# Kernel optimization log

Hardware: AMD Instinct MI355X
Metric: run time of the kernel (lower is better)

## Reference

```python
import jax, jax.numpy as jnp
import numpy as np

# Mamba2 defaults with d_model=512, headdim=2*d_model (=> nheads=1)
D_MODEL = 512
D_INNER = 2 * D_MODEL          # expand=2
D_STATE = 128
NHEADS = 1                     # d_inner // headdim = 1
HEADDIM = D_INNER              # headdim = 2*hidden_dim
D_CONV = 4
NG = 1                         # ngroups
EPS = 1e-5


def setup_inputs() -> dict:
    key = jax.random.key(0)
    ks = jax.random.split(key, 8)
    B, L = 4, 2048
    d_in_proj = 2 * D_INNER + 2 * NG * D_STATE + NHEADS   # 2305
    conv_ch = D_INNER + 2 * NG * D_STATE                  # 1280
    x = jax.random.normal(ks[0], (B, L, D_MODEL), jnp.float32)
    rnn_state = jax.random.normal(ks[1], (B, D_MODEL), jnp.float32)
    W_in = jax.random.normal(ks[2], (d_in_proj, D_MODEL), jnp.float32) * (D_MODEL ** -0.5)
    conv_w = jax.random.normal(ks[3], (conv_ch, 1, D_CONV), jnp.float32) * (D_CONV ** -0.5)
    conv_b = jnp.zeros((conv_ch,), jnp.float32)
    # dt_bias = inv_softplus(dt) with dt ~ U(1e-3, 0.1), as in Mamba2 init
    dt = jax.random.uniform(ks[4], (NHEADS,), jnp.float32, 1e-3, 0.1)
    dt_bias = jnp.log(jnp.expm1(dt))
    A_log = jnp.log(jax.random.uniform(ks[5], (NHEADS,), jnp.float32, 1.0, 16.0))
    Dp = jnp.ones((NHEADS,), jnp.float32)
    norm_w = jnp.ones((D_INNER,), jnp.float32)
    W_out = jax.random.normal(ks[6], (D_MODEL, D_INNER), jnp.float32) * (D_INNER ** -0.5)
    return dict(x=x, rnn_state=rnn_state, W_in=W_in, conv_w=conv_w, conv_b=conv_b,
                dt_bias=dt_bias, A_log=A_log, Dp=Dp, norm_w=norm_w, W_out=W_out)


def _mamba2(x, W_in, conv_w, conv_b, dt_bias, A_log, Dp, norm_w, W_out):
    B, L, _ = x.shape
    zxbcdt = jnp.einsum('bld,ed->ble', x, W_in)           # (B,L,2305)
    z, xBC, dt = jnp.split(zxbcdt, [D_INNER, 2 * D_INNER + 2 * NG * D_STATE], axis=-1)
    # causal depthwise conv1d over channels (B,C,L), then silu
    xBC = xBC.transpose(0, 2, 1)
    xBC = jax.lax.conv_general_dilated(
        xBC, conv_w, window_strides=(1,), padding=[(D_CONV - 1, 0)],
        feature_group_count=xBC.shape[1], dimension_numbers=('NCH', 'OIH', 'NCH'))
    xBC = jax.nn.silu(xBC + conv_b[None, :, None]).transpose(0, 2, 1)
    xs, Bm, Cm = jnp.split(xBC, [D_INNER, D_INNER + NG * D_STATE], axis=-1)
    xs = xs.reshape(B, L, NHEADS, HEADDIM)
    dt = jax.nn.softplus(dt + dt_bias)                    # (B,L,H)
    A = -jnp.exp(A_log)                                   # (H,)
    dA = jnp.exp(dt * A)                                  # (B,L,H)

    # selective state-space scan: h_t = dA_t*h_{t-1} + dt_t * x_t (x) B_t ; y_t = h_t @ C_t
    def step(state, inp):
        x_t, dt_t, dA_t, B_t, C_t = inp
        state = dA_t[:, :, None, None] * state \
            + (dt_t[:, :, None] * x_t)[..., None] * B_t[:, None, None, :]
        y_t = jnp.einsum('bhpn,bn->bhp', state, C_t)
        return state, y_t

    init = jnp.zeros((B, NHEADS, HEADDIM, D_STATE), x.dtype)
    inputs = (xs.transpose(1, 0, 2, 3), dt.transpose(1, 0, 2), dA.transpose(1, 0, 2),
              Bm.transpose(1, 0, 2), Cm.transpose(1, 0, 2))
    _, ys = jax.lax.scan(step, init, inputs)              # (L,B,H,P)
    y = ys.transpose(1, 0, 2, 3) + Dp[None, None, :, None] * xs
    y = y.reshape(B, L, D_INNER)
    # gated RMSNorm (gate first, norm_before_gate=False)
    y = y * jax.nn.silu(z)
    y = y * jax.lax.rsqrt(jnp.mean(y * y, axis=-1, keepdims=True) + EPS) * norm_w
    return jnp.einsum('bld,od->blo', y, W_out)


def reference(x, rnn_state, W_in, conv_w, conv_b, dt_bias, A_log, Dp, norm_w, W_out):
    out = _mamba2(x, W_in, conv_w, conv_b, dt_bias, A_log, Dp, norm_w, W_out)
    return (out, rnn_state)
```

## Files before the change

kernel.cpp:

```cpp
#include <hip/hip_runtime.h>
#include <cstdint>
#include <cstddef>


typedef __bf16 bf16_t;
typedef __bf16 bf16x8 __attribute__((ext_vector_type(8)));
typedef __bf16 bf16x4 __attribute__((ext_vector_type(4)));
typedef __bf16 bf16x2 __attribute__((ext_vector_type(2)));
typedef float  f32x4  __attribute__((ext_vector_type(4)));

#define BATCH   4
#define SEQLEN  2048
#define MROWS   8192
#define DMODEL  512
#define DINNER  1024
#define DSTATE  128
#define NZX     2304
#define NCONV   1280
#define CHUNK   128
#define NCHUNK  16
#define NBC     64

__device__ __forceinline__ float siluf(float x) { return x / (1.f + __expf(-x)); }

__device__ __forceinline__ void load_lds16(const bf16_t* g, bf16_t* l)
{
    __builtin_amdgcn_global_load_lds(
        (const __attribute__((address_space(1))) void*)g,
        (__attribute__((address_space(3))) void*)l,
        16, 0, 0);
}

template <typename OutT>
__device__ __forceinline__ void gemm_body(
    const bf16_t* __restrict__ A, const bf16_t* __restrict__ B,
    OutT* __restrict__ C, int Ntot, int K, int lda, int ldb, int bn, int bm)
{
    __shared__ __align__(16) bf16_t As[128 * 64];
    __shared__ __align__(16) bf16_t Bs[128 * 64];

    const int tid  = threadIdx.x;
    const int wave = tid >> 6, lane = tid & 63;
    const int lr = lane & 15, q = lane >> 4;
    const int wm = (wave & 1) * 64, wn = (wave >> 1) * 64;

    f32x4 acc[4][4];
    #pragma unroll
    for (int i = 0; i < 4; ++i)
        #pragma unroll
        for (int j = 0; j < 4; ++j)
            acc[i][j] = (f32x4){0.f, 0.f, 0.f, 0.f};

    const int row_a0 = bm * 128, row_b0 = bn * 128;
    const int srow = tid >> 3;
    const int gsw  = (((tid & 7) ^ (srow & 7))) * 8;
    const int lsl  = (tid & 7) * 8;

    for (int kt = 0; kt < K; kt += 64) {
        #pragma unroll
        for (int i = 0; i < 4; ++i) {
            int row = srow + i * 32;
            load_lds16(&A[(size_t)(row_a0 + row) * lda + kt + gsw], &As[row * 64 + lsl]);
            load_lds16(&B[(size_t)(row_b0 + row) * ldb + kt + gsw], &Bs[row * 64 + lsl]);
        }
        __syncthreads();
        #pragma unroll
        for (int k0 = 0; k0 < 64; k0 += 32) {
            bf16x8 af[4], bfr[4];
            #pragma unroll
            for (int mi = 0; mi < 4; ++mi) {
                int r = wm + mi * 16 + lr, kc = (k0 >> 3) + q;
                af[mi] = *reinterpret_cast<const bf16x8*>(
                    &As[r * 64 + ((kc ^ (r & 7)) << 3)]);
            }
            #pragma unroll
            for (int ni = 0; ni < 4; ++ni) {
                int r = wn + ni * 16 + lr, kc = (k0 >> 3) + q;
                bfr[ni] = *reinterpret_cast<const bf16x8*>(
                    &Bs[r * 64 + ((kc ^ (r & 7)) << 3)]);
            }
            #pragma unroll
            for (int mi = 0; mi < 4; ++mi)
                #pragma unroll
                for (int ni = 0; ni < 4; ++ni)
                    acc[mi][ni] = __builtin_amdgcn_mfma_f32_16x16x32_bf16(
                        af[mi], bfr[ni], acc[mi][ni], 0, 0, 0);
        }
        __syncthreads();
    }

    #pragma unroll
    for (int mi = 0; mi < 4; ++mi)
        #pragma unroll
        for (int ni = 0; ni < 4; ++ni)
            #pragma unroll
            for (int ri = 0; ri < 4; ++ri) {
                int row = row_a0 + wm + mi * 16 + q * 4 + ri;
                int col = row_b0 + wn + ni * 16 + lr;
                C[(size_t)row * Ntot + col] = (OutT)acc[mi][ni][ri];
            }
}

template <typename OutT>
__global__ __launch_bounds__(256) void gemm_bt_kernel(
    const bf16_t* __restrict__ A, const bf16_t* __restrict__ B,
    OutT* __restrict__ C, int Ntot, int K, int lda, int ldb,
    size_t sA, size_t sB, size_t sC)
{
    gemm_body<OutT>(A + (size_t)blockIdx.z * sA, B + (size_t)blockIdx.z * sB,
                    C + (size_t)blockIdx.z * sC, Ntot, K, lda, ldb,
                    blockIdx.x, blockIdx.y);
}

__device__ __forceinline__ void cumsum_body(
    const float* __restrict__ dtv, const float* __restrict__ A_log,
    float* __restrict__ sarr, float* __restrict__ Pv,
    float* __restrict__ EdTv, float* __restrict__ chp, int bc)
{
    __shared__ float w0sum, stot;
    int j = threadIdx.x;
    bool active = j < CHUNK;
    int lane = j & 63;
    int r = bc * CHUNK + j;
    float A = -expf(A_log[0]);
    float dt = active ? dtv[r] : 0.f;
    float s = dt;
    #pragma unroll
    for (int m = 1; m <= 32; m <<= 1) {
        float o = __shfl_up(s, m);
        if (lane >= m) s += o;
    }
    if (j == 63) w0sum = s;
    __syncthreads();
    if (j >= 64 && active) s += w0sum;
    if (j == 127) stot = s;
    __syncthreads();
    if (active) {
        float sT = stot;
        sarr[r] = s;
        Pv[r]   = expf(A * s);
        EdTv[r] = expf(A * (sT - s)) * dt;
        if (j == 127) chp[bc] = expf(A * sT);
    }
}

__global__ __launch_bounds__(256) void gemm1_kernel(
    const bf16_t* __restrict__ xb, const bf16_t* __restrict__ winb,
    bf16_t* __restrict__ zx, const float* __restrict__ dtv,
    const float* __restrict__ A_log, float* __restrict__ sarr,
    float* __restrict__ Pv, float* __restrict__ EdTv, float* __restrict__ chp)
{
    int linear = blockIdx.x;
    if (linear < (NZX / 128) * (MROWS / 128)) {
        int xcd = linear & 7, j = linear >> 3;
        int bm = xcd * 8 + (j & 7);
        int bn = j >> 3;
        gemm_body<bf16_t>(xb, winb, zx, NZX, DMODEL, DMODEL, DMODEL, bn, bm);
    } else {
        cumsum_body(dtv, A_log, sarr, Pv, EdTv, chp, linear - 1152);
    }
}

__global__ __launch_bounds__(256) void gemm2_kernel(
    const bf16_t* __restrict__ yb, const bf16_t* __restrict__ woutb,
    float* __restrict__ out)
{
    int linear = blockIdx.x;
    int xcd = linear & 7, j = linear >> 3;
    int bm = xcd * 8 + (j & 7);
    int bn = j >> 3;
    gemm_body<float>(yb, woutb, out, DMODEL, DINNER, DINNER, DINNER, bn, bm);
}

__global__ __launch_bounds__(256) void gemm_y_kernel(
    const bf16_t* __restrict__ Mx, const bf16_t* __restrict__ Xt,
    const bf16_t* __restrict__ Stb, bf16_t* __restrict__ yf)
{
    __shared__ __align__(16) bf16_t As[128 * 64];
    __shared__ __align__(16) bf16_t Bs[128 * 64];

    const int bc = blockIdx.z, bn = blockIdx.x;
    const bf16_t* Ab = Mx + (size_t)bc * 32768;
    const bf16_t* Xb = Xt  + (size_t)bc * 131072 + (size_t)bn * 128 * 128;
    const bf16_t* Sb = Stb + (size_t)bc * 131072 + (size_t)bn * 128 * 128;
    bf16_t* Cb = yf + (size_t)bc * 131072;

    const int tid  = threadIdx.x;
    const int wave = tid >> 6, lane = tid & 63;
    const int lr = lane & 15, q = lane >> 4;
    const int wm = (wave & 1) * 64, wn = (wave >> 1) * 64;

    f32x4 acc[4][4];
    #pragma unroll
    for (int i = 0; i < 4; ++i)
        #pragma unroll
        for (int j = 0; j < 4; ++j)
            acc[i][j] = (f32x4){0.f, 0.f, 0.f, 0.f};

    const int srow = tid >> 3;
    const int gsw  = (((tid & 7) ^ (srow & 7))) * 8;
    const int lsl  = (tid & 7) * 8;

    for (int kt = 0; kt < 256; kt += 64) {
        const bf16_t* bsrc = (kt < 128) ? (Xb + kt) : (Sb + (kt - 128));
        #pragma unroll
        for (int i = 0; i < 4; ++i) {
            int row = srow + i * 32;
            load_lds16(&Ab[(size_t)row * 256 + kt + gsw], &As[row * 64 + lsl]);
            load_lds16(&bsrc[(size_t)row * 128 + gsw], &Bs[row * 64 + lsl]);
        }
        __syncthreads();
        #pragma unroll
        for (int k0 = 0; k0 < 64; k0 += 32) {
            bf16x8 af[4], bfr[4];
            #pragma unroll
            for (int mi = 0; mi < 4; ++mi) {
                int r = wm + mi * 16 + lr, kc = (k0 >> 3) + q;
                af[mi] = *reinterpret_cast<const bf16x8*>(
                    &As[r * 64 + ((kc ^ (r & 7)) << 3)]);
            }
            #pragma unroll
            for (int ni = 0; ni < 4; ++ni) {
                int r = wn + ni * 16 + lr, kc = (k0 >> 3) + q;
                bfr[ni] = *reinterpret_cast<const bf16x8*>(
                    &Bs[r * 64 + ((kc ^ (r & 7)) << 3)]);
            }
            #pragma unroll
            for (int mi = 0; mi < 4; ++mi)
                #pragma unroll
                for (int ni = 0; ni < 4; ++ni)
                    acc[mi][ni] = __builtin_amdgcn_mfma_f32_16x16x32_bf16(
                        af[mi], bfr[ni], acc[mi][ni], 0, 0, 0);
        }
        __syncthreads();
    }

    #pragma unroll
    for (int mi = 0; mi < 4; ++mi)
        #pragma unroll
        for (int ni = 0; ni < 4; ++ni)
            #pragma unroll
            for (int ri = 0; ri < 4; ++ri) {
                int row = wm + mi * 16 + q * 4 + ri;
                int col = bn * 128 + wn + ni * 16 + lr;
                Cb[(size_t)row * 1024 + col] = (bf16_t)acc[mi][ni][ri];
            }
}

__global__ __launch_bounds__(256) void dtcast_kernel(
    const float* __restrict__ x, const float* __restrict__ W_in,
    const float* __restrict__ dt_bias, const float* __restrict__ W_out,
    float* __restrict__ dtv, bf16_t* __restrict__ xb,
    bf16_t* __restrict__ winb, bf16_t* __restrict__ woutb)
{
    int bid = blockIdx.x;
    if (bid < MROWS / 4) {
        int wave = threadIdx.x >> 6, lane = threadIdx.x & 63;
        int r = bid * 4 + wave;
        const float* xr = x + (size_t)r * DMODEL + lane * 8;
        const float* wr = W_in + (size_t)NZX * DMODEL + lane * 8;
        float4 a0 = *reinterpret_cast<const float4*>(xr);
        float4 a1 = *reinterpret_cast<const float4*>(xr + 4);
        float4 b0 = *reinterpret_cast<const float4*>(wr);
        float4 b1 = *reinterpret_cast<const float4*>(wr + 4);

        bf16x8 xo;
        xo[0] = (bf16_t)a0.x; xo[1] = (bf16_t)a0.y; xo[2] = (bf16_t)a0.z; xo[3] = (bf16_t)a0.w;
        xo[4] = (bf16_t)a1.x; xo[5] = (bf16_t)a1.y; xo[6] = (bf16_t)a1.z; xo[7] = (bf16_t)a1.w;
        *reinterpret_cast<bf16x8*>(xb + (size_t)r * DMODEL + lane * 8) = xo;

        float s = a0.x * b0.x + a0.y * b0.y + a0.z * b0.z + a0.w * b0.w
                + a1.x * b1.x + a1.y * b1.y + a1.z * b1.z + a1.w * b1.w;
        #pragma unroll
        for (int m = 32; m >= 1; m >>= 1) s += __shfl_xor(s, m);
        if (lane == 0) {
            float t  = s + dt_bias[0];
            dtv[r] = (t > 20.f) ? t : log1pf(expf(t));
        }
        return;
    }
    int i = (bid - MROWS / 4) * 256 + threadIdx.x;
    const int n4a = 2305 * DMODEL / 4, n4b = DMODEL * DINNER / 4;
    const float* src; bf16_t* dst; int j;
    if (i < n4a)            { src = W_in;  dst = winb;  j = i; }
    else if (i < n4a + n4b) { src = W_out; dst = woutb; j = i - n4a; }
    else return;
    float4 v = reinterpret_cast<const float4*>(src)[j];
    bf16x4 o;
    o[0] = (bf16_t)v.x; o[1] = (bf16_t)v.y; o[2] = (bf16_t)v.z; o[3] = (bf16_t)v.w;
    reinterpret_cast<bf16x4*>(dst)[j] = o;
}

__global__ __launch_bounds__(256) void conv_tr_kernel(
    const bf16_t* __restrict__ zx, const float* __restrict__ cw,
    const float* __restrict__ cb, const float* __restrict__ EdTv,
    bf16_t* __restrict__ xbc, bf16_t* __restrict__ Xt, bf16_t* __restrict__ Bwt)
{
    constexpr int TS = 66;
    __shared__ bf16_t tile[128 * TS];
    __shared__ float cwS[64 * 4];
    __shared__ float cbS[64];

    int id  = blockIdx.x;
    int xcd = id & 7;
    int k   = id >> 3;
    int bc  = xcd * 8 + (k & 7);
    int rest = k >> 3;
    int cg   = rest >> 1;
    int half = rest & 1;
    int c0   = cg * 128 + half * 64;
    int tid  = threadIdx.x;

    if (tid < 64) {
        float4 w = *reinterpret_cast<const float4*>(cw + (size_t)(c0 + tid) * 4);
        *reinterpret_cast<float4*>(&cwS[tid * 4]) = w;
        cbS[tid] = cb[c0 + tid];
    }
    __syncthreads();

    int lrow = tid >> 3;
    int lc8  = (tid & 7) * 8;
    int g0 = bc * 128;

    #pragma unroll
    for (int pass = 0; pass < 4; ++pass) {
        int row = pass * 32 + lrow;
        int g = g0 + row;
        int l = g & (SEQLEN - 1);
        float acc[8];
        #pragma unroll
        for (int m = 0; m < 8; ++m) acc[m] = cbS[lc8 + m];
        #pragma unroll
        for (int kk = 0; kk < 4; ++kk) {
            if (l + kk >= 3) {
                bf16x8 v = *reinterpret_cast<const bf16x8*>(
                    zx + (size_t)(g + kk - 3) * NZX + DINNER + c0 + lc8);
                #pragma unroll
                for (int m = 0; m < 8; ++m)
                    acc[m] += cwS[(lc8 + m) * 4 + kk] * (float)v[m];
            }
        }
        bf16x8 o;
        #pragma unroll
        for (int m = 0; m < 8; ++m) o[m] = (bf16_t)siluf(acc[m]);
        *reinterpret_cast<bf16x8*>(xbc + (size_t)g * NCONV + c0 + lc8) = o;
        if (cg < 9) {
            #pragma unroll
            for (int jj = 0; jj < 4; ++jj) {
                bf16x2 p; p[0] = o[jj * 2]; p[1] = o[jj * 2 + 1];
                *reinterpret_cast<bf16x2*>(&tile[row * TS + lc8 + jj * 2]) = p;
            }
        }
    }
    if (cg == 9) return;
    __syncthreads();

    const bool isB = (cg == 8);
    int jo = (tid >> 4) * 8;
    int i  = tid & 15;
    float sc[8];
    #pragma unroll
    for (int m = 0; m < 8; ++m)
        sc[m] = isB ? EdTv[bc * 128 + jo + m] : 1.f;

    #pragma unroll
    for (int pass = 0; pass < 4; ++pass) {
        int oc = pass * 16 + i;
        bf16x8 o;
        #pragma unroll
        for (int m = 0; m < 8; ++m)
            o[m] = (bf16_t)((float)tile[(jo + m) * TS + oc] * sc[m]);
        bf16_t* dst = isB
            ? (Bwt + (size_t)bc * 16384 + (size_t)(c0 - 1024 + oc) * 128 + jo)
            : (Xt + (size_t)bc * 131072 + (size_t)(c0 + oc) * 128 + jo);
        *reinterpret_cast<bf16x8*>(dst) = o;
    }
}

__global__ __launch_bounds__(256) void scan_combine_kernel(
    const bf16_t* __restrict__ cstate, const float* __restrict__ chp,
    bf16_t* __restrict__ Stb)
{
    int idx = blockIdx.x * 256 + threadIdx.x;
    int b   = idx >> 17;
    int np  = idx & 131071;
    float v = 0.f;
    for (int c = 0; c < NCHUNK; ++c) {
        size_t off = ((size_t)(b * NCHUNK + c) << 17) + np;
        Stb[off] = (bf16_t)v;
        float tmp = (float)cstate[off];
        v = chp[b * NCHUNK + c] * v + tmp;
    }
}

__global__ __launch_bounds__(256) void mbuild_kernel(
    const float* __restrict__ sarr, const float* __restrict__ dtv,
    const float* __restrict__ Pv, const float* __restrict__ A_log,
    const bf16_t* __restrict__ xbc, bf16_t* __restrict__ Mx)
{
    __shared__ __align__(16) bf16_t Cs[128 * 128];
    __shared__ __align__(16) bf16_t Bs2[128 * 128];
    __shared__ float sj[CHUNK], dj[CHUNK], pj[CHUNK];

    int bc = blockIdx.x, tid = threadIdx.x;
    if (tid < CHUNK) {
        sj[tid] = sarr[bc * CHUNK + tid];
        dj[tid] = dtv[bc * CHUNK + tid];
        pj[tid] = Pv[bc * CHUNK + tid];
    }
    int rowbase = bc * 128;
    int srow = tid >> 4;
    int gsw  = (((tid & 15) ^ (srow & 7))) * 8;
    int lsl  = (tid & 15) * 8;
    #pragma unroll
    for (int i = 0; i < 8; ++i) {
        int row = srow + i * 16;
        load_lds16(&xbc[(size_t)(rowbase + row) * NCONV + 1152 + gsw], &Cs[row * 128 + lsl]);
        load_lds16(&xbc[(size_t)(rowbase + row) * NCONV + 1024 + gsw], &Bs2[row * 128 + lsl]);
    }
    __syncthreads();

    const int wave = tid >> 6, lane = tid & 63;
    const int lr = lane & 15, q = lane >> 4;
    const int wm = (wave & 1) * 64, wn = (wave >> 1) * 64;

    f32x4 acc[4][4];
    #pragma unroll
    for (int i = 0; i < 4; ++i)
        #pragma unroll
        for (int j = 0; j < 4; ++j)
            acc[i][j] = (f32x4){0.f, 0.f, 0.f, 0.f};

    #pragma unroll
    for (int k0 = 0; k0 < 128; k0 += 32) {
        bf16x8 af[4], bfr[4];
        #pragma unroll
        for (int mi = 0; mi < 4; ++mi) {
            int r = wm + mi * 16 + lr, kc = (k0 >> 3) + q;
            af[mi] = *reinterpret_cast<const bf16x8*>(
                &Cs[r * 128 + ((kc ^ (r & 7)) << 3)]);
        }
        #pragma unroll
        for (int ni = 0; ni < 4; ++ni) {
            int r = wn + ni * 16 + lr, kc = (k0 >> 3) + q;
            bfr[ni] = *reinterpret_cast<const bf16x8*>(
                &Bs2[r * 128 + ((kc ^ (r & 7)) << 3)]);
        }
        #pragma unroll
        for (int mi = 0; mi < 4; ++mi)
            #pragma unroll
            for (int ni = 0; ni < 4; ++ni)
                acc[mi][ni] = __builtin_amdgcn_mfma_f32_16x16x32_bf16(
                    af[mi], bfr[ni], acc[mi][ni], 0, 0, 0);
    }

    float A = -expf(A_log[0]);
    bf16_t* MxB = Mx + (size_t)bc * 32768;
    #pragma unroll
    for (int mi = 0; mi < 4; ++mi)
        #pragma unroll
        for (int ni = 0; ni < 4; ++ni)
            #pragma unroll
            for (int ri = 0; ri < 4; ++ri) {
                int row = wm + mi * 16 + q * 4 + ri;
                int col = wn + ni * 16 + lr;
                float val = 0.f;
                if (col <= row)
                    val = acc[mi][ni][ri] * expf(A * (sj[row] - sj[col])) * dj[col];
                MxB[(size_t)row * 256 + col] = (bf16_t)val;
            }

    int rr = tid >> 1, cb2 = (tid & 1) * 64;
    float Pi = pj[rr];
    #pragma unroll
    for (int m0 = 0; m0 < 64; m0 += 8) {
        int kc = (cb2 + m0) >> 3;
        bf16x8 cv = *reinterpret_cast<const bf16x8*>(
            &Cs[rr * 128 + ((kc ^ (rr & 7)) << 3)]);
        bf16x8 o;
        #pragma unroll
        for (int m = 0; m < 8; ++m) o[m] = (bf16_t)((float)cv[m] * Pi);
        *reinterpret_cast<bf16x8*>(&MxB[(size_t)rr * 256 + 128 + cb2 + m0]) = o;
    }
}

__global__ __launch_bounds__(256) void gate_norm_kernel(
    const bf16_t* __restrict__ yf, const bf16_t* __restrict__ zx,
    const bf16_t* __restrict__ xbc, const float* __restrict__ Dp,
    const float* __restrict__ norm_w, bf16_t* __restrict__ yb,
    const float* __restrict__ rnn, float* __restrict__ outTail)
{
    __shared__ float red[4];
    int r = blockIdx.x, tid = threadIdx.x;
    if (r >= MROWS) {
        int i = (r - MROWS) * 256 + tid;
        if (i < BATCH * DMODEL) outTail[i] = rnn[i];
        return;
    }
    int p = tid * 4;
    float D0 = Dp[0];
    bf16x4 yv = *reinterpret_cast<const bf16x4*>(yf + (size_t)r * DINNER + p);
    bf16x4 zv = *reinterpret_cast<const bf16x4*>(zx + (size_t)r * NZX + p);
    bf16x4 xv = *reinterpret_cast<const bf16x4*>(xbc + (size_t)r * NCONV + p);
    float g0 = ((float)yv[0] + D0 * (float)xv[0]) * siluf((float)zv[0]);
    float g1 = ((float)yv[1] + D0 * (float)xv[1]) * siluf((float)zv[1]);
    float g2 = ((float)yv[2] + D0 * (float)xv[2]) * siluf((float)zv[2]);
    float g3 = ((float)yv[3] + D0 * (float)xv[3]) * siluf((float)zv[3]);
    float ss = g0 * g0 + g1 * g1 + g2 * g2 + g3 * g3;
    #pragma unroll
    for (int m = 32; m >= 1; m >>= 1) ss += __shfl_xor(ss, m);
    if ((tid & 63) == 0) red[tid >> 6] = ss;
    __syncthreads();
    float tot = red[0] + red[1] + red[2] + red[3];
    float scale = rsqrtf(tot * (1.f / 1024.f) + 1e-5f);
    float4 nw = *reinterpret_cast<const float4*>(norm_w + p);
    bf16x4 o;
    o[0] = (bf16_t)(g0 * scale * nw.x);
    o[1] = (bf16_t)(g1 * scale * nw.y);
    o[2] = (bf16_t)(g2 * scale * nw.z);
    o[3] = (bf16_t)(g3 * scale * nw.w);
    *reinterpret_cast<bf16x4*>(yb + (size_t)r * DINNER + p) = o;
}

extern "C" void kernel_launch(void* const* d_in, const int* in_sizes, int n_in,
                              void* d_out, int out_size, void* d_ws, size_t ws_size,
                              hipStream_t stream)
{
    const float* x        = (const float*)d_in[0];
    const float* rnn      = (const float*)d_in[1];
    const float* W_in     = (const float*)d_in[2];
    const float* conv_w   = (const float*)d_in[3];
    const float* conv_b   = (const float*)d_in[4];
    const float* dt_bias  = (const float*)d_in[5];
    const float* A_log    = (const float*)d_in[6];
    const float* Dp       = (const float*)d_in[7];
    const float* norm_w   = (const float*)d_in[8];
    const float* W_out    = (const float*)d_in[9];
    float* out = (float*)d_out;

    char* ws = (char*)d_ws;
    bf16_t* xb     = (bf16_t*)(ws + 0);
    bf16_t* Mx     = (bf16_t*)(ws + 4194304);
    bf16_t* winb   = (bf16_t*)(ws + 8388608);
    bf16_t* woutb  = (bf16_t*)(ws + 10748928);
    bf16_t* zx     = (bf16_t*)(ws + 11797504);
    float*  dtv    = (float*) (ws + 49546240);
    float*  sarr   = (float*) (ws + 49579008);
    float*  Pv     = (float*) (ws + 49611776);
    float*  EdTv   = (float*) (ws + 49644544);
    float*  chp    = (float*) (ws + 49677312);
    bf16_t* xbcb   = (bf16_t*)(ws + 49677568);
    bf16_t* Xt     = (bf16_t*)(ws + 70649088);
    bf16_t* Bwt    = (bf16_t*)(ws + 87426304);
    bf16_t* cstate = (bf16_t*)(ws + 89523456);
    bf16_t* yf     = (bf16_t*)(ws + 89523456);
    bf16_t* Stb    = (bf16_t*)(ws + 106300672);
    bf16_t* yb     = (bf16_t*)(ws + 123077888);

    {
        const int n4a = 2305 * DMODEL / 4, n4b = DMODEL * DINNER / 4;
        int grid = MROWS / 4 + (n4a + n4b + 255) / 256;
        dtcast_kernel<<<grid, 256, 0, stream>>>(
            x, W_in, dt_bias, W_out, dtv, xb, winb, woutb);
    }

    gemm1_kernel<<<1152 + NBC, 256, 0, stream>>>(
        xb, winb, zx, dtv, A_log, sarr, Pv, EdTv, chp);

    conv_tr_kernel<<<1280, 256, 0, stream>>>(
        zx, conv_w, conv_b, EdTv, xbcb, Xt, Bwt);

    gemm_bt_kernel<bf16_t><<<dim3(1, 8, NBC), 256, 0, stream>>>(
        Xt, Bwt, cstate, DSTATE, CHUNK, CHUNK, CHUNK,
        131072, 16384, 131072);

    scan_combine_kernel<<<BATCH * 131072 / 256, 256, 0, stream>>>(cstate, chp, Stb);

    mbuild_kernel<<<NBC, 256, 0, stream>>>(sarr, dtv, Pv, A_log, xbcb, Mx);

    gemm_y_kernel<<<dim3(8, 1, NBC), 256, 0, stream>>>(Mx, Xt, Stb, yf);

    gate_norm_kernel<<<MROWS + 8, 256, 0, stream>>>(
        yf, zx, xbcb, Dp, norm_w, yb, rnn, out + (size_t)MROWS * DMODEL);

    gemm2_kernel<<<256, 256, 0, stream>>>(yb, woutb, out);
}
```

Before: 219.0 us.

## Fuse chunk-state GEMM with mbuild, batch scan loads, wave-per-row gate norm

```diff
diff --git a/kernel.cpp b/kernel.cpp
--- a/kernel.cpp
+++ b/kernel.cpp
@@ -33,11 +33,12 @@
 
 template <typename OutT>
 __device__ __forceinline__ void gemm_body(
+    unsigned char* smem,
     const bf16_t* __restrict__ A, const bf16_t* __restrict__ B,
     OutT* __restrict__ C, int Ntot, int K, int lda, int ldb, int bn, int bm)
 {
-    __shared__ __align__(16) bf16_t As[128 * 64];
-    __shared__ __align__(16) bf16_t Bs[128 * 64];
+    bf16_t* As = (bf16_t*)smem;
+    bf16_t* Bs = (bf16_t*)(smem + 16384);
 
     const int tid  = threadIdx.x;
     const int wave = tid >> 6, lane = tid & 63;
@@ -99,17 +100,6 @@
                 int col = row_b0 + wn + ni * 16 + lr;
                 C[(size_t)row * Ntot + col] = (OutT)acc[mi][ni][ri];
             }
-}
-
-template <typename OutT>
-__global__ __launch_bounds__(256) void gemm_bt_kernel(
-    const bf16_t* __restrict__ A, const bf16_t* __restrict__ B,
-    OutT* __restrict__ C, int Ntot, int K, int lda, int ldb,
-    size_t sA, size_t sB, size_t sC)
-{
-    gemm_body<OutT>(A + (size_t)blockIdx.z * sA, B + (size_t)blockIdx.z * sB,
-                    C + (size_t)blockIdx.z * sC, Ntot, K, lda, ldb,
-                    blockIdx.x, blockIdx.y);
 }
 
 __device__ __forceinline__ void cumsum_body(
@@ -150,12 +140,13 @@
     const float* __restrict__ A_log, float* __restrict__ sarr,
     float* __restrict__ Pv, float* __restrict__ EdTv, float* __restrict__ chp)
 {
+    __shared__ __align__(16) unsigned char smem[32768];
     int linear = blockIdx.x;
     if (linear < (NZX / 128) * (MROWS / 128)) {
         int xcd = linear & 7, j = linear >> 3;
         int bm = xcd * 8 + (j & 7);
         int bn = j >> 3;
-        gemm_body<bf16_t>(xb, winb, zx, NZX, DMODEL, DMODEL, DMODEL, bn, bm);
+        gemm_body<bf16_t>(smem, xb, winb, zx, NZX, DMODEL, DMODEL, DMODEL, bn, bm);
     } else {
         cumsum_body(dtv, A_log, sarr, Pv, EdTv, chp, linear - 1152);
     }
@@ -165,11 +156,126 @@
     const bf16_t* __restrict__ yb, const bf16_t* __restrict__ woutb,
     float* __restrict__ out)
 {
+    __shared__ __align__(16) unsigned char smem[32768];
     int linear = blockIdx.x;
     int xcd = linear & 7, j = linear >> 3;
     int bm = xcd * 8 + (j & 7);
     int bn = j >> 3;
-    gemm_body<float>(yb, woutb, out, DMODEL, DINNER, DINNER, DINNER, bn, bm);
+    gemm_body<float>(smem, yb, woutb, out, DMODEL, DINNER, DINNER, DINNER, bn, bm);
+}
+
+__device__ __forceinline__ void mbuild_body(
+    unsigned char* smem,
+    const float* __restrict__ sarr, const float* __restrict__ dtv,
+    const float* __restrict__ Pv, const float* __restrict__ A_log,
+    const bf16_t* __restrict__ xbc, bf16_t* __restrict__ Mx, int bc)
+{
+    bf16_t* Cs  = (bf16_t*)smem;
+    bf16_t* Bs2 = (bf16_t*)(smem + 32768);
+    float* sj = (float*)(smem + 65536);
+    float* dj = (float*)(smem + 65536 + 512);
+    float* pj = (float*)(smem + 65536 + 1024);
+
+    int tid = threadIdx.x;
+    if (tid < CHUNK) {
+        sj[tid] = sarr[bc * CHUNK + tid];
+        dj[tid] = dtv[bc * CHUNK + tid];
+        pj[tid] = Pv[bc * CHUNK + tid];
+    }
+    int rowbase = bc * 128;
+    int srow = tid >> 4;
+    int gsw  = (((tid & 15) ^ (srow & 7))) * 8;
+    int lsl  = (tid & 15) * 8;
+    #pragma unroll
+    for (int i = 0; i < 8; ++i) {
+        int row = srow + i * 16;
+        load_lds16(&xbc[(size_t)(rowbase + row) * NCONV + 1152 + gsw], &Cs[row * 128 + lsl]);
+        load_lds16(&xbc[(size_t)(rowbase + row) * NCONV + 1024 + gsw], &Bs2[row * 128 + lsl]);
+    }
+    __syncthreads();
+
+    const int wave = tid >> 6, lane = tid & 63;
+    const int lr = lane & 15, q = lane >> 4;
+    const int wm = (wave & 1) * 64, wn = (wave >> 1) * 64;
+
+    f32x4 acc[4][4];
+    #pragma unroll
+    for (int i = 0; i < 4; ++i)
+        #pragma unroll
+        for (int j = 0; j < 4; ++j)
+            acc[i][j] = (f32x4){0.f, 0.f, 0.f, 0.f};
+
+    #pragma unroll
+    for (int k0 = 0; k0 < 128; k0 += 32) {
+        bf16x8 af[4], bfr[4];
+        #pragma unroll
+        for (int mi = 0; mi < 4; ++mi) {
+            int r = wm + mi * 16 + lr, kc = (k0 >> 3) + q;
+            af[mi] = *reinterpret_cast<const bf16x8*>(
+                &Cs[r * 128 + ((kc ^ (r & 7)) << 3)]);
+        }
+        #pragma unroll
+        for (int ni = 0; ni < 4; ++ni) {
+            int r = wn + ni * 16 + lr, kc = (k0 >> 3) + q;
+            bfr[ni] = *reinterpret_cast<const bf16x8*>(
+                &Bs2[r * 128 + ((kc ^ (r & 7)) << 3)]);
+        }
+        #pragma unroll
+        for (int mi = 0; mi < 4; ++mi)
+            #pragma unroll
+            for (int ni = 0; ni < 4; ++ni)
+                acc[mi][ni] = __builtin_amdgcn_mfma_f32_16x16x32_bf16(
+                    af[mi], bfr[ni], acc[mi][ni], 0, 0, 0);
+    }
+
+    float A = -expf(A_log[0]);
+    bf16_t* MxB = Mx + (size_t)bc * 32768;
+    #pragma unroll
+    for (int mi = 0; mi < 4; ++mi)
+        #pragma unroll
+        for (int ni = 0; ni < 4; ++ni)
+            #pragma unroll
+            for (int ri = 0; ri < 4; ++ri) {
+                int row = wm + mi * 16 + q * 4 + ri;
+                int col = wn + ni * 16 + lr;
+                float val = 0.f;
+                if (col <= row)
+                    val = acc[mi][ni][ri] * expf(A * (sj[row] - sj[col])) * dj[col];
+                MxB[(size_t)row * 256 + col] = (bf16_t)val;
+            }
+
+    int rr = tid >> 1, cb2 = (tid & 1) * 64;
+    float Pi = pj[rr];
+    #pragma unroll
+    for (int m0 = 0; m0 < 64; m0 += 8) {
+        int kc = (cb2 + m0) >> 3;
+        bf16x8 cv = *reinterpret_cast<const bf16x8*>(
+            &Cs[rr * 128 + ((kc ^ (rr & 7)) << 3)]);
+        bf16x8 o;
+        #pragma unroll
+        for (int m = 0; m < 8; ++m) o[m] = (bf16_t)((float)cv[m] * Pi);
+        *reinterpret_cast<bf16x8*>(&MxB[(size_t)rr * 256 + 128 + cb2 + m0]) = o;
+    }
+}
+
+__global__ __launch_bounds__(256) void gemmA_mbuild_kernel(
+    const bf16_t* __restrict__ Xt, const bf16_t* __restrict__ Bwt,
+    bf16_t* __restrict__ cstate,
+    const float* __restrict__ sarr, const float* __restrict__ dtv,
+    const float* __restrict__ Pv, const float* __restrict__ A_log,
+    const bf16_t* __restrict__ xbc, bf16_t* __restrict__ Mx)
+{
+    __shared__ __align__(16) unsigned char smem[67072];
+    int id = blockIdx.x;
+    if (id < 512) {
+        int bc = id & 63, bm = id >> 6;
+        gemm_body<bf16_t>(smem,
+            Xt + (size_t)bc * 131072, Bwt + (size_t)bc * 16384,
+            cstate + (size_t)bc * 131072,
+            DSTATE, CHUNK, CHUNK, CHUNK, 0, bm);
+    } else {
+        mbuild_body(smem, sarr, dtv, Pv, A_log, xbc, Mx, id - 512);
+    }
 }
 
 __global__ __launch_bounds__(256) void gemm_y_kernel(
@@ -381,106 +487,23 @@
     const bf16_t* __restrict__ cstate, const float* __restrict__ chp,
     bf16_t* __restrict__ Stb)
 {
+    __shared__ float chS[NCHUNK];
     int idx = blockIdx.x * 256 + threadIdx.x;
     int b   = idx >> 17;
     int np  = idx & 131071;
+    if (threadIdx.x < NCHUNK) chS[threadIdx.x] = chp[b * NCHUNK + threadIdx.x];
+    __syncthreads();
+
+    const bf16_t* src = cstate + ((size_t)b << 21) + np;
+    bf16_t*       dst = Stb    + ((size_t)b << 21) + np;
+    float t[NCHUNK];
+    #pragma unroll
+    for (int c = 0; c < NCHUNK; ++c) t[c] = (float)src[(size_t)c << 17];
     float v = 0.f;
+    #pragma unroll
     for (int c = 0; c < NCHUNK; ++c) {
-        size_t off = ((size_t)(b * NCHUNK + c) << 17) + np;
-        Stb[off] = (bf16_t)v;
-        float tmp = (float)cstate[off];
-        v = chp[b * NCHUNK + c] * v + tmp;
-    }
-}
-
-__global__ __launch_bounds__(256) void mbuild_kernel(
-    const float* __restrict__ sarr, const float* __restrict__ dtv,
-    const float* __restrict__ Pv, const float* __restrict__ A_log,
-    const bf16_t* __restrict__ xbc, bf16_t* __restrict__ Mx)
-{
-    __shared__ __align__(16) bf16_t Cs[128 * 128];
-    __shared__ __align__(16) bf16_t Bs2[128 * 128];
-    __shared__ float sj[CHUNK], dj[CHUNK], pj[CHUNK];
-
-    int bc = blockIdx.x, tid = threadIdx.x;
-    if (tid < CHUNK) {
-        sj[tid] = sarr[bc * CHUNK + tid];
-        dj[tid] = dtv[bc * CHUNK + tid];
-        pj[tid] = Pv[bc * CHUNK + tid];
-    }
-    int rowbase = bc * 128;
-    int srow = tid >> 4;
-    int gsw  = (((tid & 15) ^ (srow & 7))) * 8;
-    int lsl  = (tid & 15) * 8;
-    #pragma unroll
-    for (int i = 0; i < 8; ++i) {
-        int row = srow + i * 16;
-        load_lds16(&xbc[(size_t)(rowbase + row) * NCONV + 1152 + gsw], &Cs[row * 128 + lsl]);
-        load_lds16(&xbc[(size_t)(rowbase + row) * NCONV + 1024 + gsw], &Bs2[row * 128 + lsl]);
-    }
-    __syncthreads();
-
-    const int wave = tid >> 6, lane = tid & 63;
-    const int lr = lane & 15, q = lane >> 4;
-    const int wm = (wave & 1) * 64, wn = (wave >> 1) * 64;
-
-    f32x4 acc[4][4];
-    #pragma unroll
-    for (int i = 0; i < 4; ++i)
-        #pragma unroll
-        for (int j = 0; j < 4; ++j)
-            acc[i][j] = (f32x4){0.f, 0.f, 0.f, 0.f};
-
-    #pragma unroll
-    for (int k0 = 0; k0 < 128; k0 += 32) {
-        bf16x8 af[4], bfr[4];
-        #pragma unroll
-        for (int mi = 0; mi < 4; ++mi) {
-            int r = wm + mi * 16 + lr, kc = (k0 >> 3) + q;
-            af[mi] = *reinterpret_cast<const bf16x8*>(
-                &Cs[r * 128 + ((kc ^ (r & 7)) << 3)]);
-        }
-        #pragma unroll
-        for (int ni = 0; ni < 4; ++ni) {
-            int r = wn + ni * 16 + lr, kc = (k0 >> 3) + q;
-            bfr[ni] = *reinterpret_cast<const bf16x8*>(
-                &Bs2[r * 128 + ((kc ^ (r & 7)) << 3)]);
-        }
-        #pragma unroll
-        for (int mi = 0; mi < 4; ++mi)
-            #pragma unroll
-            for (int ni = 0; ni < 4; ++ni)
-                acc[mi][ni] = __builtin_amdgcn_mfma_f32_16x16x32_bf16(
-                    af[mi], bfr[ni], acc[mi][ni], 0, 0, 0);
-    }
-
-    float A = -expf(A_log[0]);
-    bf16_t* MxB = Mx + (size_t)bc * 32768;
-    #pragma unroll
-    for (int mi = 0; mi < 4; ++mi)
-        #pragma unroll
-        for (int ni = 0; ni < 4; ++ni)
-            #pragma unroll
-            for (int ri = 0; ri < 4; ++ri) {
-                int row = wm + mi * 16 + q * 4 + ri;
-                int col = wn + ni * 16 + lr;
-                float val = 0.f;
-                if (col <= row)
-                    val = acc[mi][ni][ri] * expf(A * (sj[row] - sj[col])) * dj[col];
-                MxB[(size_t)row * 256 + col] = (bf16_t)val;
-            }
-
-    int rr = tid >> 1, cb2 = (tid & 1) * 64;
-    float Pi = pj[rr];
-    #pragma unroll
-    for (int m0 = 0; m0 < 64; m0 += 8) {
-        int kc = (cb2 + m0) >> 3;
-        bf16x8 cv = *reinterpret_cast<const bf16x8*>(
-            &Cs[rr * 128 + ((kc ^ (rr & 7)) << 3)]);
-        bf16x8 o;
-        #pragma unroll
-        for (int m = 0; m < 8; ++m) o[m] = (bf16_t)((float)cv[m] * Pi);
-        *reinterpret_cast<bf16x8*>(&MxB[(size_t)rr * 256 + 128 + cb2 + m0]) = o;
+        dst[(size_t)c << 17] = (bf16_t)v;
+        v = chS[c] * v + t[c];
     }
 }
 
@@ -490,36 +513,52 @@
     const float* __restrict__ norm_w, bf16_t* __restrict__ yb,
     const float* __restrict__ rnn, float* __restrict__ outTail)
 {
-    __shared__ float red[4];
-    int r = blockIdx.x, tid = threadIdx.x;
-    if (r >= MROWS) {
-        int i = (r - MROWS) * 256 + tid;
+    int blk = blockIdx.x, tid = threadIdx.x;
+    if (blk >= MROWS / 4) {
+        int i = (blk - MROWS / 4) * 256 + tid;
         if (i < BATCH * DMODEL) outTail[i] = rnn[i];
         return;
     }
-    int p = tid * 4;
+    int wave = tid >> 6, lane = tid & 63;
+    int r = blk * 4 + wave;
+    int p0 = lane * 8, p1 = 512 + lane * 8;
     float D0 = Dp[0];
-    bf16x4 yv = *reinterpret_cast<const bf16x4*>(yf + (size_t)r * DINNER + p);
-    bf16x4 zv = *reinterpret_cast<const bf16x4*>(zx + (size_t)r * NZX + p);
-    bf16x4 xv = *reinterpret_cast<const bf16x4*>(xbc + (size_t)r * NCONV + p);
-    float g0 = ((float)yv[0] + D0 * (float)xv[0]) * siluf((float)zv[0]);
-    float g1 = ((float)yv[1] + D0 * (float)xv[1]) * siluf((float)zv[1]);
-    float g2 = ((float)yv[2] + D0 * (float)xv[2]) * siluf((float)zv[2]);
-    float g3 = ((float)yv[3] + D0 * (float)xv[3]) * siluf((float)zv[3]);
-    float ss = g0 * g0 + g1 * g1 + g2 * g2 + g3 * g3;
+
+    bf16x8 y0 = *reinterpret_cast<const bf16x8*>(yf + (size_t)r * DINNER + p0);
+    bf16x8 y1 = *reinterpret_cast<const bf16x8*>(yf + (size_t)r * DINNER + p1);
+    bf16x8 z0 = *reinterpret_cast<const bf16x8*>(zx + (size_t)r * NZX + p0);
+    bf16x8 z1 = *reinterpret_cast<const bf16x8*>(zx + (size_t)r * NZX + p1);
+    bf16x8 x0 = *reinterpret_cast<const bf16x8*>(xbc + (size_t)r * NCONV + p0);
+    bf16x8 x1 = *reinterpret_cast<const bf16x8*>(xbc + (size_t)r * NCONV + p1);
+
+    float g[16];
+    #pragma unroll
+    for (int m = 0; m < 8; ++m) {
+        g[m]     = ((float)y0[m] + D0 * (float)x0[m]) * siluf((float)z0[m]);
+        g[8 + m] = ((float)y1[m] + D0 * (float)x1[m]) * siluf((float)z1[m]);
+    }
+    float ss = 0.f;
+    #pragma unroll
+    for (int m = 0; m < 16; ++m) ss += g[m] * g[m];
     #pragma unroll
     for (int m = 32; m >= 1; m >>= 1) ss += __shfl_xor(ss, m);
-    if ((tid & 63) == 0) red[tid >> 6] = ss;
-    __syncthreads();
-    float tot = red[0] + red[1] + red[2] + red[3];
-    float scale = rsqrtf(tot * (1.f / 1024.f) + 1e-5f);
-    float4 nw = *reinterpret_cast<const float4*>(norm_w + p);
-    bf16x4 o;
-    o[0] = (bf16_t)(g0 * scale * nw.x);
-    o[1] = (bf16_t)(g1 * scale * nw.y);
-    o[2] = (bf16_t)(g2 * scale * nw.z);
-    o[3] = (bf16_t)(g3 * scale * nw.w);
-    *reinterpret_cast<bf16x4*>(yb + (size_t)r * DINNER + p) = o;
+    float scale = rsqrtf(ss * (1.f / 1024.f) + 1e-5f);
+
+    const float* nw = norm_w;
+    float4 w0a = *reinterpret_cast<const float4*>(nw + p0);
+    float4 w0b = *reinterpret_cast<const float4*>(nw + p0 + 4);
+    float4 w1a = *reinterpret_cast<const float4*>(nw + p1);
+    float4 w1b = *reinterpret_cast<const float4*>(nw + p1 + 4);
+    float w[16] = {w0a.x, w0a.y, w0a.z, w0a.w, w0b.x, w0b.y, w0b.z, w0b.w,
+                   w1a.x, w1a.y, w1a.z, w1a.w, w1b.x, w1b.y, w1b.z, w1b.w};
+    bf16x8 o0, o1;
+    #pragma unroll
+    for (int m = 0; m < 8; ++m) {
+        o0[m] = (bf16_t)(g[m] * scale * w[m]);
+        o1[m] = (bf16_t)(g[8 + m] * scale * w[8 + m]);
+    }
+    *reinterpret_cast<bf16x8*>(yb + (size_t)r * DINNER + p0) = o0;
+    *reinterpret_cast<bf16x8*>(yb + (size_t)r * DINNER + p1) = o1;
 }
 
 extern "C" void kernel_launch(void* const* d_in, const int* in_sizes, int n_in,
@@ -570,17 +609,14 @@
     conv_tr_kernel<<<1280, 256, 0, stream>>>(
         zx, conv_w, conv_b, EdTv, xbcb, Xt, Bwt);
 
-    gemm_bt_kernel<bf16_t><<<dim3(1, 8, NBC), 256, 0, stream>>>(
-        Xt, Bwt, cstate, DSTATE, CHUNK, CHUNK, CHUNK,
-        131072, 16384, 131072);
+    gemmA_mbuild_kernel<<<576, 256, 0, stream>>>(
+        Xt, Bwt, cstate, sarr, dtv, Pv, A_log, xbcb, Mx);
 
     scan_combine_kernel<<<BATCH * 131072 / 256, 256, 0, stream>>>(cstate, chp, Stb);
 
-    mbuild_kernel<<<NBC, 256, 0, stream>>>(sarr, dtv, Pv, A_log, xbcb, Mx);
-
     gemm_y_kernel<<<dim3(8, 1, NBC), 256, 0, stream>>>(Mx, Xt, Stb, yf);
 
-    gate_norm_kernel<<<MROWS + 8, 256, 0, stream>>>(
+    gate_norm_kernel<<<MROWS / 4 + 8, 256, 0, stream>>>(
         yf, zx, xbcb, Dp, norm_w, yb, rnn, out + (size_t)MROWS * DMODEL);
 
     gemm2_kernel<<<256, 256, 0, stream>>>(yb, woutb, out);
```

Result: faster. 214.0 us (-2.3%).
